# Optimization experiments

Hardware: AMD Instinct MI355X
Metric: run time of the kernel (lower is better)

## Reference

```python
import jax, jax.numpy as jnp
import numpy as np

D_MODEL = 5
NUM_PRED = 3
D_K = D_MODEL + NUM_PRED  # 8
HIDDEN = 128
GRID_LEN = 0.1
NUM_GRIDS = 100  # time_horizon / grid_length
SCALE = float(np.power(D_K, 0.5))
OH = np.eye(NUM_PRED, dtype=np.float32)
ONEHOT_M = jnp.asarray(OH[0])   # mental predicate 0
ONEHOT_A1 = jnp.asarray(OH[1])  # action predicate 1
ONEHOT_A2 = jnp.asarray(OH[2])  # action predicate 2


def time_emb(t):
    # positional-style embedding: even dims sin, odd dims cos (matches fast_time_embedding)
    i = jnp.arange(D_MODEL)
    ang = jnp.asarray(t)[..., None] / (10000.0 ** (2.0 * i / D_MODEL))
    return jnp.where(i % 2 == 0, jnp.sin(ang), jnp.cos(ang))


def setup_inputs() -> dict:
    key = jax.random.key(0)
    ks = jax.random.split(key, 11)
    B, L = 1024, 2048
    times_a1 = jnp.sort(jax.random.uniform(ks[0], (B, L)) * 10.0, axis=1)
    times_a2 = jnp.sort(jax.random.uniform(ks[1], (B, L)) * 10.0, axis=1)
    u = jax.random.uniform(ks[2], (B, NUM_GRIDS))
    s = 0.05
    return {
        'times_a1': times_a1,
        'times_a2': times_a2,
        'u': u,
        'W_ih': s * jax.random.normal(ks[3], (4 * HIDDEN, 21)),
        'W_hh': s * jax.random.normal(ks[4], (4 * HIDDEN, HIDDEN)),
        'b_ih': s * jax.random.normal(ks[5], (4 * HIDDEN,)),
        'b_hh': s * jax.random.normal(ks[6], (4 * HIDDEN,)),
        'w1': s * jax.random.normal(ks[7], (5, HIDDEN)),
        'b1': s * jax.random.normal(ks[8], (5,)),
        'w2': s * jax.random.normal(ks[9], (1, 5)),
        'b2': s * jax.random.normal(ks[10], (1,)),
    }


def _forward(times_a1, times_a2, u, W_ih, W_hh, b_ih, b_hh, w1, b1, w2, b2):
    B = times_a1.shape[0]
    # action event embeddings: [B, L, D_MODEL+NUM_PRED]; k = v = concat over action types
    e1 = jnp.concatenate([time_emb(times_a1), jnp.broadcast_to(ONEHOT_A1, times_a1.shape + (NUM_PRED,))], axis=-1)
    e2 = jnp.concatenate([time_emb(times_a2), jnp.broadcast_to(ONEHOT_A2, times_a2.shape + (NUM_PRED,))], axis=-1)
    kv = jnp.concatenate([e1, e2], axis=1)  # [B, 2L, 8]

    cur_times = (jnp.arange(NUM_GRIDS) + 1.0) * GRID_LEN  # [100]

    def step(carry, xs):
        hx, cx, last_time, has_event, dyn_time = carry
        cur_time, u_t = xs
        # query for mental predicate 0 at cur_time: [8]
        q = jnp.concatenate([time_emb(cur_time), ONEHOT_M])
        scores = jnp.einsum('d,bld->bl', q, kv) / SCALE
        attn = jax.nn.softmax(scores, axis=-1)
        att_out = jnp.einsum('bl,bld->bd', attn, kv)  # [B, 8]
        # mental embedding: zeros before first event, else time-emb of last event + one-hot
        m_emb = jnp.concatenate([time_emb(last_time), jnp.broadcast_to(ONEHOT_M, (B, NUM_PRED))], axis=-1)
        m_emb = jnp.where(has_event[:, None], m_emb, 0.0)
        dyn_time = dyn_time + GRID_LEN
        ct_emb = time_emb(dyn_time)  # [B, 5]
        x = jnp.concatenate([att_out, m_emb, ct_emb], axis=-1)  # [B, 21]
        # torch LSTMCell: gates ordered i, f, g, o
        gates = x @ W_ih.T + hx @ W_hh.T + b_ih + b_hh
        i_, f_, g_, o_ = jnp.split(gates, 4, axis=-1)
        cx = jax.nn.sigmoid(f_) * cx + jax.nn.sigmoid(i_) * jnp.tanh(g_)
        hx = jax.nn.sigmoid(o_) * jnp.tanh(cx)
        hz = jax.nn.sigmoid((hx @ w1.T + b1) @ w2.T + b2)[:, 0]  # [B]
        # bernoulli(prob) with pre-drawn uniform; single mental predicate -> index always 0
        event = u_t < hz
        last_time = jnp.where(event, cur_time, last_time)
        has_event = has_event | event
        dyn_time = jnp.where(event, 0.0, dyn_time)
        return (hx, cx, last_time, has_event, dyn_time), (hz, event)

    init = (
        jnp.zeros((B, HIDDEN)), jnp.zeros((B, HIDDEN)),
        jnp.zeros((B,)), jnp.zeros((B,), dtype=bool), jnp.zeros((B,)),
    )
    _, (hazard, events) = jax.lax.scan(step, init, (cur_times, u.T))
    return hazard, events  # [NUM_GRIDS, B], [NUM_GRIDS, B]


def reference(times_a1, times_a2, u, W_ih, W_hh, b_ih, b_hh, w1, b1, w2, b2):
    return _forward(times_a1, times_a2, u, W_ih, W_hh, b_ih, b_hh, w1, b1, w2, b2)
```

## Files before the change

### kernel.cpp

```cpp
#include <hip/hip_runtime.h>
#include <math.h>

#define BTOT 1024
#define LEN  2048
#define T    100
#define HID  128

#define C1 0.025118864315095794
#define C2 6.309573444801933e-04
#define C3 1.5848931924611134e-05
#define C4 3.9810717055349735e-07

#define TEMB(td) \
  float d0 = sinf((float)(td)); \
  float d1 = cosf((float)((td) * C1)); \
  float d2 = sinf((float)((td) * C2)); \
  float d3 = cosf((float)((td) * C3)); \
  float d4 = sinf((float)((td) * C4));

__device__ __forceinline__ float sig(float x) { return 1.0f / (1.0f + expf(-x)); }

template <int CTRL>
__device__ __forceinline__ float dppadd(float x) {
  int r = __builtin_amdgcn_update_dpp(0, __float_as_int(x), CTRL, 0xF, 0xF, false);
  return x + __int_as_float(r);
}
__device__ __forceinline__ float wred(float x) {
  x = dppadd<0xB1>(x);
  x = dppadd<0x4E>(x);
  x = dppadd<0x124>(x);
  x = dppadd<0x128>(x);
  x += __shfl_xor(x, 16);
  x += __shfl_xor(x, 32);
  return x;
}

__global__ __launch_bounds__(256)
__attribute__((amdgpu_waves_per_eu(4, 4)))
void attn_k(const float* __restrict__ ta1,
            const float* __restrict__ ta2,
            float* __restrict__ att) {
  const int b = blockIdx.x, tid = threadIdx.x;
  const int wave = tid >> 6, lane = tid & 63;

  __shared__ float qlds[T][8];
  __shared__ float strip[4][T][8];

  if (tid < T) {
    double ct = (double)(tid + 1) * 0.1;
    TEMB(ct);
    qlds[tid][0] = d0 * 0.35355339059327373f;
    qlds[tid][1] = d1 * 0.35355339059327373f;
    qlds[tid][2] = d2 * 0.35355339059327373f;
    qlds[tid][3] = d3 * 0.35355339059327373f;
    qlds[tid][4] = d4 * 0.35355339059327373f;
  }

#define E5(i) float e##i##_0, e##i##_1, e##i##_2, e##i##_3, e##i##_4;
  E5(0) E5(1) E5(2) E5(3) E5(4) E5(5) E5(6) E5(7)
  E5(8) E5(9) E5(10) E5(11) E5(12) E5(13) E5(14) E5(15)
#undef E5
#define STAGE(i, expr) { double td_ = (double)(expr); \
    e##i##_0 = sinf((float)td_); \
    e##i##_1 = cosf((float)(td_ * C1)); \
    e##i##_2 = sinf((float)(td_ * C2)); \
    e##i##_3 = cosf((float)(td_ * C3)); \
    e##i##_4 = sinf((float)(td_ * C4)); }
  STAGE(0,  ta1[b * LEN + tid +    0])
  STAGE(1,  ta1[b * LEN + tid +  256])
  STAGE(2,  ta1[b * LEN + tid +  512])
  STAGE(3,  ta1[b * LEN + tid +  768])
  STAGE(4,  ta1[b * LEN + tid + 1024])
  STAGE(5,  ta1[b * LEN + tid + 1280])
  STAGE(6,  ta1[b * LEN + tid + 1536])
  STAGE(7,  ta1[b * LEN + tid + 1792])
  STAGE(8,  ta2[b * LEN + tid +    0])
  STAGE(9,  ta2[b * LEN + tid +  256])
  STAGE(10, ta2[b * LEN + tid +  512])
  STAGE(11, ta2[b * LEN + tid +  768])
  STAGE(12, ta2[b * LEN + tid + 1024])
  STAGE(13, ta2[b * LEN + tid + 1280])
  STAGE(14, ta2[b * LEN + tid + 1536])
  STAGE(15, ta2[b * LEN + tid + 1792])
#undef STAGE
#define PIN5(i) asm volatile("" : "+v"(e##i##_0), "+v"(e##i##_1), \
    "+v"(e##i##_2), "+v"(e##i##_3), "+v"(e##i##_4));
  PIN5(0) PIN5(1) PIN5(2) PIN5(3) PIN5(4) PIN5(5) PIN5(6) PIN5(7)
  PIN5(8) PIN5(9) PIN5(10) PIN5(11) PIN5(12) PIN5(13) PIN5(14) PIN5(15)
#undef PIN5

  __syncthreads();

  for (int t = 0; t < T; t++) {
    const float4 qv = *(const float4*)&qlds[t][0];
    const float q4 = qlds[t][4];
    float Wx = 0.f, Wy = 0.f, Wz = 0.f, Ww = 0.f, W4 = 0.f, sA = 0.f, sB = 0.f;
#define EV(i, S) { \
    float s = fmaf(qv.x, e##i##_0, fmaf(qv.y, e##i##_1, \
              fmaf(qv.z, e##i##_2, fmaf(qv.w, e##i##_3, q4 * e##i##_4)))); \
    float e = __expf(s); S += e; \
    Wx = fmaf(e, e##i##_0, Wx); Wy = fmaf(e, e##i##_1, Wy); \
    Wz = fmaf(e, e##i##_2, Wz); Ww = fmaf(e, e##i##_3, Ww); \
    W4 = fmaf(e, e##i##_4, W4); }
    EV(0, sA) EV(1, sA) EV(2, sA) EV(3, sA)
    EV(4, sA) EV(5, sA) EV(6, sA) EV(7, sA)
    EV(8, sB) EV(9, sB) EV(10, sB) EV(11, sB)
    EV(12, sB) EV(13, sB) EV(14, sB) EV(15, sB)
#undef EV

    float r0 = wred(Wx), r1 = wred(Wy), r2 = wred(Wz), r3 = wred(Ww);
    float r4 = wred(W4), r5 = wred(sA), r6 = wred(sB);
    if (lane == 0) {
      *(float4*)&strip[wave][t][0] = make_float4(r0, r1, r2, r3);
      strip[wave][t][4] = r4; strip[wave][t][5] = r5; strip[wave][t][6] = r6;
    }
  }
  __syncthreads();

  if (tid < T) {
    float4 a0 = *(float4*)&strip[0][tid][0], b0 = *(float4*)&strip[0][tid][4];
    float4 a1 = *(float4*)&strip[1][tid][0], b1 = *(float4*)&strip[1][tid][4];
    float4 a2 = *(float4*)&strip[2][tid][0], b2 = *(float4*)&strip[2][tid][4];
    float4 a3 = *(float4*)&strip[3][tid][0], b3 = *(float4*)&strip[3][tid][4];
    float f0 = a0.x + a1.x + a2.x + a3.x;
    float f1 = a0.y + a1.y + a2.y + a3.y;
    float f2 = a0.z + a1.z + a2.z + a3.z;
    float f3 = a0.w + a1.w + a2.w + a3.w;
    float f4 = b0.x + b1.x + b2.x + b3.x;
    float f5 = b0.y + b1.y + b2.y + b3.y;
    float f6 = b0.z + b1.z + b2.z + b3.z;
    float inv = 1.0f / (f5 + f6);
    float* o8 = &att[(size_t)b * (T * 8) + (size_t)tid * 8];
    o8[0] = f0 * inv; o8[1] = f1 * inv; o8[2] = f2 * inv;
    o8[3] = f3 * inv; o8[4] = f4 * inv;
    o8[5] = 0.f; o8[6] = f5 * inv; o8[7] = f6 * inv;
  }
}

__device__ __forceinline__ float wcat(const float* Wih, const float* Whh, int r, int e) {
  return (e < 21) ? Wih[r * 21 + e] : (e < 24) ? 0.f : Whh[r * HID + e - 24];
}

__global__ __launch_bounds__(1024)
__attribute__((amdgpu_waves_per_eu(4, 4)))
void lstm_k(const float* __restrict__ att,
            const float* __restrict__ u,
            const float* __restrict__ Wih,
            const float* __restrict__ Whh,
            const float* __restrict__ bih,
            const float* __restrict__ bhh,
            const float* __restrict__ w1g,
            const float* __restrict__ b1g,
            const float* __restrict__ w2g,
            const float* __restrict__ b2g,
            float* __restrict__ out) {
  const int tid = threadIdx.x;
  const int bg = blockIdx.x * 4;
  const int r = tid >> 1, half = tid & 1;
  const int CB = 19 * half;
  const int ch = tid & 127;

  __shared__ float4 xb4[4 * 38];
  __shared__ float glf[4 * 512];
  __shared__ float red[8][5];
  __shared__ int stL[2][4], stD[2][4], stH[2][4];
  float* xbf = (float*)xb4;

  const int eb = 76 * half;
#define DECLW(c) float wr##c##_0 = wcat(Wih, Whh, r, eb + 4*(c) + 0), \
                       wr##c##_1 = wcat(Wih, Whh, r, eb + 4*(c) + 1), \
                       wr##c##_2 = wcat(Wih, Whh, r, eb + 4*(c) + 2), \
                       wr##c##_3 = wcat(Wih, Whh, r, eb + 4*(c) + 3);
  DECLW(0) DECLW(1) DECLW(2) DECLW(3) DECLW(4) DECLW(5) DECLW(6) DECLW(7)
  DECLW(8) DECLW(9) DECLW(10) DECLW(11) DECLW(12) DECLW(13) DECLW(14)
  DECLW(15) DECLW(16) DECLW(17) DECLW(18)
#undef DECLW
  float binit = half ? 0.f : (bih[r] + bhh[r]);

  float w1_0 = w1g[0*HID + ch], w1_1 = w1g[1*HID + ch], w1_2 = w1g[2*HID + ch],
        w1_3 = w1g[3*HID + ch], w1_4 = w1g[4*HID + ch];
  const float b1_0 = b1g[0], b1_1 = b1g[1], b1_2 = b1g[2], b1_3 = b1g[3], b1_4 = b1g[4];
  const float w2_0 = w2g[0], w2_1 = w2g[1], w2_2 = w2g[2], w2_3 = w2g[3], w2_4 = w2g[4];
  const float b2r = b2g[0];

#define PINW(c) asm volatile("" : "+v"(wr##c##_0), "+v"(wr##c##_1), \
    "+v"(wr##c##_2), "+v"(wr##c##_3));
  PINW(0) PINW(1) PINW(2) PINW(3) PINW(4) PINW(5) PINW(6) PINW(7)
  PINW(8) PINW(9) PINW(10) PINW(11) PINW(12) PINW(13) PINW(14)
  PINW(15) PINW(16) PINW(17) PINW(18)
#undef PINW
  asm volatile("" : "+v"(binit), "+v"(w1_0), "+v"(w1_1), "+v"(w1_2),
                    "+v"(w1_3), "+v"(w1_4));

  for (int i = tid; i < 4 * 152; i += 1024) xbf[i] = 0.f;
  if (tid < 4) { stL[0][tid] = 0; stD[0][tid] = 0; stH[0][tid] = 0; }
  float cx = 0.f;
  __syncthreads();

  if (tid < 32) {
    int b = tid >> 3, j = tid & 7;
    xbf[b * 152 + j] = att[(size_t)(bg + b) * (T * 8) + j];
  } else if (tid >= 64 && tid < 84) {
    int s = tid - 64, b = s / 5, j = s % 5;
    TEMB(0.1);
    xbf[b * 152 + 16 + j] = (j == 0) ? d0 : (j == 1) ? d1 : (j == 2) ? d2 : (j == 3) ? d3 : d4;
  }
  __syncthreads();

#define CALCEV(bb) \
    float z_ = b2r; \
    z_ = fmaf(w2_0, red[2*(bb)][0] + red[2*(bb)+1][0] + b1_0, z_); \
    z_ = fmaf(w2_1, red[2*(bb)][1] + red[2*(bb)+1][1] + b1_1, z_); \
    z_ = fmaf(w2_2, red[2*(bb)][2] + red[2*(bb)+1][2] + b1_2, z_); \
    z_ = fmaf(w2_3, red[2*(bb)][3] + red[2*(bb)+1][3] + b1_3, z_); \
    z_ = fmaf(w2_4, red[2*(bb)][4] + red[2*(bb)+1][4] + b1_4, z_); \
    float hz_ = 1.f / (1.f + expf(-z_)); \
    int ev_ = (u[(size_t)(bg + (bb)) * T + t] < hz_) ? 1 : 0; \
    int tb_ = t & 1; \
    int lastp_ = ev_ ? (t + 1) : stL[tb_][bb]; \
    int hasp_ = stH[tb_][bb] | ev_; \
    int dynp_ = ev_ ? 0 : (stD[tb_][bb] + 1);

  for (int t = 0; t < T; t++) {
    float a0 = binit, a1 = binit, a2 = binit, a3 = binit;
#define GB(c) { \
    float4 v0 = xb4[0*38 + CB + (c)], v1 = xb4[1*38 + CB + (c)]; \
    float4 v2 = xb4[2*38 + CB + (c)], v3 = xb4[3*38 + CB + (c)]; \
    a0 = fmaf(wr##c##_0, v0.x, a0); a0 = fmaf(wr##c##_1, v0.y, a0); \
    a0 = fmaf(wr##c##_2, v0.z, a0); a0 = fmaf(wr##c##_3, v0.w, a0); \
    a1 = fmaf(wr##c##_0, v1.x, a1); a1 = fmaf(wr##c##_1, v1.y, a1); \
    a1 = fmaf(wr##c##_2, v1.z, a1); a1 = fmaf(wr##c##_3, v1.w, a1); \
    a2 = fmaf(wr##c##_0, v2.x, a2); a2 = fmaf(wr##c##_1, v2.y, a2); \
    a2 = fmaf(wr##c##_2, v2.z, a2); a2 = fmaf(wr##c##_3, v2.w, a2); \
    a3 = fmaf(wr##c##_0, v3.x, a3); a3 = fmaf(wr##c##_1, v3.y, a3); \
    a3 = fmaf(wr##c##_2, v3.z, a3); a3 = fmaf(wr##c##_3, v3.w, a3); }
    GB(0) GB(1) GB(2) GB(3) GB(4) GB(5) GB(6) GB(7) GB(8) GB(9)
    GB(10) GB(11) GB(12) GB(13) GB(14) GB(15) GB(16) GB(17) GB(18)
#undef GB
    a0 = dppadd<0xB1>(a0); a1 = dppadd<0xB1>(a1);
    a2 = dppadd<0xB1>(a2); a3 = dppadd<0xB1>(a3);
    if (!half) {
      glf[0*512 + r] = a0; glf[1*512 + r] = a1;
      glf[2*512 + r] = a2; glf[3*512 + r] = a3;
    }
    __syncthreads();

    if (tid < 512) {
      int b = tid >> 7;
      float gi = glf[b*512 + ch], gf = glf[b*512 + 128 + ch],
            gg = glf[b*512 + 256 + ch], go = glf[b*512 + 384 + ch];
      cx = sig(gf) * cx + sig(gi) * tanhf(gg);
      float hn = sig(go) * tanhf(cx);
      xbf[b * 152 + 24 + ch] = hn;
      float p0 = wred(w1_0 * hn), p1 = wred(w1_1 * hn), p2 = wred(w1_2 * hn),
            p3 = wred(w1_3 * hn), p4 = wred(w1_4 * hn);
      if ((tid & 63) == 0) {
        int w = tid >> 6;
        red[w][0] = p0; red[w][1] = p1; red[w][2] = p2;
        red[w][3] = p3; red[w][4] = p4;
      }
    }
    __syncthreads();

    if (tid < 4) {
      int b = tid;
      CALCEV(b);
      out[(size_t)t * BTOT + bg + b] = hz_;
      out[(size_t)T * BTOT + (size_t)t * BTOT + bg + b] = ev_ ? 1.f : 0.f;
      stL[tb_ ^ 1][b] = lastp_; stH[tb_ ^ 1][b] = hasp_; stD[tb_ ^ 1][b] = dynp_;
    }
    if (t < T - 1) {
      if (tid < 32) {
        int b = tid >> 3, j = tid & 7;
        xbf[b * 152 + j] = att[(size_t)(bg + b) * (T * 8) + (size_t)(t + 1) * 8 + j];
      } else if (tid < 52) {
        int s = tid - 32, b = s / 5, j = s % 5;
        CALCEV(b);
        float v = 0.f;
        if (hasp_) {
          double td = (double)lastp_ * 0.1;
          TEMB(td);
          v = (j == 0) ? d0 : (j == 1) ? d1 : (j == 2) ? d2 : (j == 3) ? d3 : d4;
        }
        xbf[b * 152 + 8 + j] = v;
      } else if (tid < 64) {
        int s = tid - 52, b = s / 3, j = s % 3;
        CALCEV(b);
        xbf[b * 152 + 13 + j] = (j == 0 && hasp_) ? 1.f : 0.f;
      } else if (tid < 84) {
        int s = tid - 64, b = s / 5, j = s % 5;
        CALCEV(b);
        double td = (double)(dynp_ + 1) * 0.1;
        TEMB(td);
        xbf[b * 152 + 16 + j] =
            (j == 0) ? d0 : (j == 1) ? d1 : (j == 2) ? d2 : (j == 3) ? d3 : d4;
      }
    }
    __syncthreads();
  }
#undef CALCEV
}

extern "C" void kernel_launch(void* const* d_in, const int* in_sizes, int n_in,
                              void* d_out, int out_size, void* d_ws, size_t ws_size,
                              hipStream_t stream) {
  const float* ta1 = (const float*)d_in[0];
  const float* ta2 = (const float*)d_in[1];
  const float* u   = (const float*)d_in[2];
  const float* Wih = (const float*)d_in[3];
  const float* Whh = (const float*)d_in[4];
  const float* bih = (const float*)d_in[5];
  const float* bhh = (const float*)d_in[6];
  const float* w1  = (const float*)d_in[7];
  const float* b1  = (const float*)d_in[8];
  const float* w2  = (const float*)d_in[9];
  const float* b2  = (const float*)d_in[10];
  float* out = (float*)d_out;
  float* att = (float*)d_ws;

  attn_k<<<dim3(BTOT), dim3(256), 0, stream>>>(ta1, ta2, att);
  lstm_k<<<dim3(BTOT / 4), dim3(1024), 0, stream>>>(att, u, Wih, Whh, bih, bhh,
                                                    w1, b1, w2, b2, out);
}
```

Measured before the change: 836.9 us.

## Restructure LSTM step so each thread owns all four gates of one unit

```diff
diff --git a/kernel.cpp b/kernel.cpp
--- a/kernel.cpp
+++ b/kernel.cpp
@@ -19,6 +19,9 @@
   float d4 = sinf((float)((td) * C4));
 
 __device__ __forceinline__ float sig(float x) { return 1.0f / (1.0f + expf(-x)); }
+
+using v2f = __attribute__((ext_vector_type(2))) float;
+__device__ __forceinline__ v2f mkv2(float a, float b) { v2f r; r.x = a; r.y = b; return r; }
 
 template <int CTRL>
 __device__ __forceinline__ float dppadd(float x) {
@@ -34,9 +37,9 @@
   x += __shfl_xor(x, 32);
   return x;
 }
-
-__global__ __launch_bounds__(256)
-__attribute__((amdgpu_waves_per_eu(4, 4)))
+#define RED8(x) { x = dppadd<0xB1>(x); x = dppadd<0x4E>(x); x = dppadd<0x141>(x); }
+
+__global__ __attribute__((amdgpu_flat_work_group_size(256, 256), amdgpu_waves_per_eu(4, 4)))
 void attn_k(const float* __restrict__ ta1,
             const float* __restrict__ ta2,
             float* __restrict__ att) {
@@ -137,12 +140,16 @@
   }
 }
 
-__device__ __forceinline__ float wcat(const float* Wih, const float* Whh, int r, int e) {
-  return (e < 21) ? Wih[r * 21 + e] : (e < 24) ? 0.f : Whh[r * HID + e - 24];
-}
-
-__global__ __launch_bounds__(1024)
-__attribute__((amdgpu_waves_per_eu(4, 4)))
+__device__ __forceinline__ float wc(const float* Wih, const float* Whh, int row, int e) {
+  return (e < 21) ? Wih[row * 21 + e]
+       : (e < 24) ? 0.f
+       : (e < 152) ? Whh[row * HID + (e - 24)]
+       : 0.f;
+}
+
+#define XE(tb, b, e) (((tb) * 4 + (b)) * 160 + (e))
+
+__global__ __attribute__((amdgpu_flat_work_group_size(1024, 1024), amdgpu_waves_per_eu(4, 4)))
 void lstm_k(const float* __restrict__ att,
             const float* __restrict__ u,
             const float* __restrict__ Wih,
@@ -156,109 +163,115 @@
             float* __restrict__ out) {
   const int tid = threadIdx.x;
   const int bg = blockIdx.x * 4;
-  const int r = tid >> 1, half = tid & 1;
-  const int CB = 19 * half;
-  const int ch = tid & 127;
-
-  __shared__ float4 xb4[4 * 38];
-  __shared__ float glf[4 * 512];
-  __shared__ float red[8][5];
+  const int q = tid >> 3, s = tid & 7;
+  const int wave = tid >> 6, lane = tid & 63;
+
+  __shared__ float4 xls4[2][4][40];
+  __shared__ float4 red4[2][4][4];
   __shared__ int stL[2][4], stD[2][4], stH[2][4];
-  float* xbf = (float*)xb4;
-
-  const int eb = 76 * half;
-#define DECLW(c) float wr##c##_0 = wcat(Wih, Whh, r, eb + 4*(c) + 0), \
-                       wr##c##_1 = wcat(Wih, Whh, r, eb + 4*(c) + 1), \
-                       wr##c##_2 = wcat(Wih, Whh, r, eb + 4*(c) + 2), \
-                       wr##c##_3 = wcat(Wih, Whh, r, eb + 4*(c) + 3);
-  DECLW(0) DECLW(1) DECLW(2) DECLW(3) DECLW(4) DECLW(5) DECLW(6) DECLW(7)
-  DECLW(8) DECLW(9) DECLW(10) DECLW(11) DECLW(12) DECLW(13) DECLW(14)
-  DECLW(15) DECLW(16) DECLW(17) DECLW(18)
-#undef DECLW
-  float binit = half ? 0.f : (bih[r] + bhh[r]);
-
-  float w1_0 = w1g[0*HID + ch], w1_1 = w1g[1*HID + ch], w1_2 = w1g[2*HID + ch],
-        w1_3 = w1g[3*HID + ch], w1_4 = w1g[4*HID + ch];
-  const float b1_0 = b1g[0], b1_1 = b1g[1], b1_2 = b1g[2], b1_3 = b1g[3], b1_4 = b1g[4];
-  const float w2_0 = w2g[0], w2_1 = w2g[1], w2_2 = w2g[2], w2_3 = w2g[3], w2_4 = w2g[4];
-  const float b2r = b2g[0];
-
-#define PINW(c) asm volatile("" : "+v"(wr##c##_0), "+v"(wr##c##_1), \
-    "+v"(wr##c##_2), "+v"(wr##c##_3));
-  PINW(0) PINW(1) PINW(2) PINW(3) PINW(4) PINW(5) PINW(6) PINW(7)
-  PINW(8) PINW(9) PINW(10) PINW(11) PINW(12) PINW(13) PINW(14)
-  PINW(15) PINW(16) PINW(17) PINW(18)
-#undef PINW
-  asm volatile("" : "+v"(binit), "+v"(w1_0), "+v"(w1_1), "+v"(w1_2),
-                    "+v"(w1_3), "+v"(w1_4));
-
-  for (int i = tid; i < 4 * 152; i += 1024) xbf[i] = 0.f;
+  float* xf = (float*)xls4;
+  float* rf = (float*)red4;
+
+#define WD(g, c) v2f w##g##_##c = mkv2(wc(Wih, Whh, q + 128 * (g), 20 * s + 2 * (c)), \
+                                       wc(Wih, Whh, q + 128 * (g), 20 * s + 2 * (c) + 1));
+#define WR(g) WD(g, 0) WD(g, 1) WD(g, 2) WD(g, 3) WD(g, 4) WD(g, 5) WD(g, 6) WD(g, 7) WD(g, 8) WD(g, 9)
+  WR(0) WR(1) WR(2) WR(3)
+#undef WR
+#undef WD
+#define PW(g) asm volatile("" : "+v"(w##g##_0), "+v"(w##g##_1), "+v"(w##g##_2), \
+    "+v"(w##g##_3), "+v"(w##g##_4), "+v"(w##g##_5), "+v"(w##g##_6), "+v"(w##g##_7), \
+    "+v"(w##g##_8), "+v"(w##g##_9));
+  PW(0) PW(1) PW(2) PW(3)
+#undef PW
+
+  float bb0 = bih[q] + bhh[q];
+  float bb1 = bih[q + 128] + bhh[q + 128];
+  float bb2 = bih[q + 256] + bhh[q + 256];
+  float bb3 = bih[q + 384] + bhh[q + 384];
+  float wv = 0.f;
+#pragma unroll
+  for (int j = 0; j < 5; j++) wv = fmaf(w2g[j], w1g[j * HID + q], wv);
+  float hconst = b2g[0];
+#pragma unroll
+  for (int j = 0; j < 5; j++) hconst = fmaf(w2g[j], b1g[j], hconst);
+  asm volatile("" : "+v"(bb0), "+v"(bb1), "+v"(bb2), "+v"(bb3), "+v"(wv));
+  float cx0 = 0.f, cx1 = 0.f, cx2 = 0.f, cx3 = 0.f;
+
+  for (int i = tid; i < 2 * 4 * 160; i += 1024) xf[i] = 0.f;
   if (tid < 4) { stL[0][tid] = 0; stD[0][tid] = 0; stH[0][tid] = 0; }
-  float cx = 0.f;
   __syncthreads();
 
   if (tid < 32) {
     int b = tid >> 3, j = tid & 7;
-    xbf[b * 152 + j] = att[(size_t)(bg + b) * (T * 8) + j];
+    xf[XE(0, b, j)] = att[(size_t)(bg + b) * (T * 8) + j];
   } else if (tid >= 64 && tid < 84) {
-    int s = tid - 64, b = s / 5, j = s % 5;
+    int s2 = tid - 64, b = s2 / 5, j = s2 % 5;
     TEMB(0.1);
-    xbf[b * 152 + 16 + j] = (j == 0) ? d0 : (j == 1) ? d1 : (j == 2) ? d2 : (j == 3) ? d3 : d4;
+    xf[XE(0, b, 16 + j)] = (j == 0) ? d0 : (j == 1) ? d1 : (j == 2) ? d2 : (j == 3) ? d3 : d4;
   }
   __syncthreads();
 
+#define FMS(g, a) \
+  a = __builtin_elementwise_fma(w##g##_0, mkv2(u0.x, u0.y), a); \
+  a = __builtin_elementwise_fma(w##g##_1, mkv2(u0.z, u0.w), a); \
+  a = __builtin_elementwise_fma(w##g##_2, mkv2(u1.x, u1.y), a); \
+  a = __builtin_elementwise_fma(w##g##_3, mkv2(u1.z, u1.w), a); \
+  a = __builtin_elementwise_fma(w##g##_4, mkv2(u2.x, u2.y), a); \
+  a = __builtin_elementwise_fma(w##g##_5, mkv2(u2.z, u2.w), a); \
+  a = __builtin_elementwise_fma(w##g##_6, mkv2(u3.x, u3.y), a); \
+  a = __builtin_elementwise_fma(w##g##_7, mkv2(u3.z, u3.w), a); \
+  a = __builtin_elementwise_fma(w##g##_8, mkv2(u4.x, u4.y), a); \
+  a = __builtin_elementwise_fma(w##g##_9, mkv2(u4.z, u4.w), a);
+
+#define BATCH(b, s0, s1, s2n, s3n) { \
+  const float4* xp = &xls4[tb][b][s * 5]; \
+  float4 u0 = xp[0], u1 = xp[1], u2 = xp[2], u3 = xp[3], u4 = xp[4]; \
+  v2f a0 = mkv2(0.f, 0.f), a1 = a0, a2 = a0, a3 = a0; \
+  FMS(0, a0) FMS(1, a1) FMS(2, a2) FMS(3, a3) \
+  s0 = a0.x + a0.y; s1 = a1.x + a1.y; s2n = a2.x + a2.y; s3n = a3.x + a3.y; }
+
+#define CELL(b, cxv) { \
+  float gi = g0##b + bb0, gf = g1##b + bb1, gG = g2##b + bb2, go = g3##b + bb3; \
+  cxv = sig(gf) * cxv + sig(gi) * tanhf(gG); \
+  float hn = sig(go) * tanhf(cxv); \
+  xf[XE(tb1, b, 24 + q)] = hn; \
+  pb##b = wv * hn; }
+
 #define CALCEV(bb) \
-    float z_ = b2r; \
-    z_ = fmaf(w2_0, red[2*(bb)][0] + red[2*(bb)+1][0] + b1_0, z_); \
-    z_ = fmaf(w2_1, red[2*(bb)][1] + red[2*(bb)+1][1] + b1_1, z_); \
-    z_ = fmaf(w2_2, red[2*(bb)][2] + red[2*(bb)+1][2] + b1_2, z_); \
-    z_ = fmaf(w2_3, red[2*(bb)][3] + red[2*(bb)+1][3] + b1_3, z_); \
-    z_ = fmaf(w2_4, red[2*(bb)][4] + red[2*(bb)+1][4] + b1_4, z_); \
+    float4 r0 = red4[tb][bb][0], r1 = red4[tb][bb][1], \
+           r2 = red4[tb][bb][2], r3 = red4[tb][bb][3]; \
+    float z_ = hconst + (((r0.x + r0.y) + (r0.z + r0.w)) + ((r1.x + r1.y) + (r1.z + r1.w))) \
+                      + (((r2.x + r2.y) + (r2.z + r2.w)) + ((r3.x + r3.y) + (r3.z + r3.w))); \
     float hz_ = 1.f / (1.f + expf(-z_)); \
     int ev_ = (u[(size_t)(bg + (bb)) * T + t] < hz_) ? 1 : 0; \
-    int tb_ = t & 1; \
-    int lastp_ = ev_ ? (t + 1) : stL[tb_][bb]; \
-    int hasp_ = stH[tb_][bb] | ev_; \
-    int dynp_ = ev_ ? 0 : (stD[tb_][bb] + 1);
+    int lastp_ = ev_ ? (t + 1) : stL[tb][bb]; \
+    int hasp_ = stH[tb][bb] | ev_; \
+    int dynp_ = ev_ ? 0 : (stD[tb][bb] + 1);
 
   for (int t = 0; t < T; t++) {
-    float a0 = binit, a1 = binit, a2 = binit, a3 = binit;
-#define GB(c) { \
-    float4 v0 = xb4[0*38 + CB + (c)], v1 = xb4[1*38 + CB + (c)]; \
-    float4 v2 = xb4[2*38 + CB + (c)], v3 = xb4[3*38 + CB + (c)]; \
-    a0 = fmaf(wr##c##_0, v0.x, a0); a0 = fmaf(wr##c##_1, v0.y, a0); \
-    a0 = fmaf(wr##c##_2, v0.z, a0); a0 = fmaf(wr##c##_3, v0.w, a0); \
-    a1 = fmaf(wr##c##_0, v1.x, a1); a1 = fmaf(wr##c##_1, v1.y, a1); \
-    a1 = fmaf(wr##c##_2, v1.z, a1); a1 = fmaf(wr##c##_3, v1.w, a1); \
-    a2 = fmaf(wr##c##_0, v2.x, a2); a2 = fmaf(wr##c##_1, v2.y, a2); \
-    a2 = fmaf(wr##c##_2, v2.z, a2); a2 = fmaf(wr##c##_3, v2.w, a2); \
-    a3 = fmaf(wr##c##_0, v3.x, a3); a3 = fmaf(wr##c##_1, v3.y, a3); \
-    a3 = fmaf(wr##c##_2, v3.z, a3); a3 = fmaf(wr##c##_3, v3.w, a3); }
-    GB(0) GB(1) GB(2) GB(3) GB(4) GB(5) GB(6) GB(7) GB(8) GB(9)
-    GB(10) GB(11) GB(12) GB(13) GB(14) GB(15) GB(16) GB(17) GB(18)
-#undef GB
-    a0 = dppadd<0xB1>(a0); a1 = dppadd<0xB1>(a1);
-    a2 = dppadd<0xB1>(a2); a3 = dppadd<0xB1>(a3);
-    if (!half) {
-      glf[0*512 + r] = a0; glf[1*512 + r] = a1;
-      glf[2*512 + r] = a2; glf[3*512 + r] = a3;
-    }
-    __syncthreads();
-
-    if (tid < 512) {
-      int b = tid >> 7;
-      float gi = glf[b*512 + ch], gf = glf[b*512 + 128 + ch],
-            gg = glf[b*512 + 256 + ch], go = glf[b*512 + 384 + ch];
-      cx = sig(gf) * cx + sig(gi) * tanhf(gg);
-      float hn = sig(go) * tanhf(cx);
-      xbf[b * 152 + 24 + ch] = hn;
-      float p0 = wred(w1_0 * hn), p1 = wred(w1_1 * hn), p2 = wred(w1_2 * hn),
-            p3 = wred(w1_3 * hn), p4 = wred(w1_4 * hn);
-      if ((tid & 63) == 0) {
-        int w = tid >> 6;
-        red[w][0] = p0; red[w][1] = p1; red[w][2] = p2;
-        red[w][3] = p3; red[w][4] = p4;
-      }
+    const int tb = t & 1, tb1 = tb ^ 1;
+
+    float g00, g10, g20, g30, g01, g11, g21, g31,
+          g02, g12, g22, g32, g03, g13, g23, g33;
+    BATCH(0, g00, g10, g20, g30)
+    BATCH(1, g01, g11, g21, g31)
+    BATCH(2, g02, g12, g22, g32)
+    BATCH(3, g03, g13, g23, g33)
+    RED8(g00) RED8(g10) RED8(g20) RED8(g30)
+    RED8(g01) RED8(g11) RED8(g21) RED8(g31)
+    RED8(g02) RED8(g12) RED8(g22) RED8(g32)
+    RED8(g03) RED8(g13) RED8(g23) RED8(g33)
+
+    float pb0 = 0.f, pb1 = 0.f, pb2 = 0.f, pb3 = 0.f;
+    if (s == 0) {
+      CELL(0, cx0) CELL(1, cx1) CELL(2, cx2) CELL(3, cx3)
+    }
+    pb0 = wred(pb0); pb1 = wred(pb1); pb2 = wred(pb2); pb3 = wred(pb3);
+    if (lane == 0) {
+      rf[(tb * 4 + 0) * 16 + wave] = pb0;
+      rf[(tb * 4 + 1) * 16 + wave] = pb1;
+      rf[(tb * 4 + 2) * 16 + wave] = pb2;
+      rf[(tb * 4 + 3) * 16 + wave] = pb3;
     }
     __syncthreads();
 
@@ -267,14 +280,14 @@
       CALCEV(b);
       out[(size_t)t * BTOT + bg + b] = hz_;
       out[(size_t)T * BTOT + (size_t)t * BTOT + bg + b] = ev_ ? 1.f : 0.f;
-      stL[tb_ ^ 1][b] = lastp_; stH[tb_ ^ 1][b] = hasp_; stD[tb_ ^ 1][b] = dynp_;
+      stL[tb1][b] = lastp_; stH[tb1][b] = hasp_; stD[tb1][b] = dynp_;
     }
     if (t < T - 1) {
       if (tid < 32) {
         int b = tid >> 3, j = tid & 7;
-        xbf[b * 152 + j] = att[(size_t)(bg + b) * (T * 8) + (size_t)(t + 1) * 8 + j];
+        xf[XE(tb1, b, j)] = att[(size_t)(bg + b) * (T * 8) + (size_t)(t + 1) * 8 + j];
       } else if (tid < 52) {
-        int s = tid - 32, b = s / 5, j = s % 5;
+        int s2 = tid - 32, b = s2 / 5, j = s2 % 5;
         CALCEV(b);
         float v = 0.f;
         if (hasp_) {
@@ -282,23 +295,26 @@
           TEMB(td);
           v = (j == 0) ? d0 : (j == 1) ? d1 : (j == 2) ? d2 : (j == 3) ? d3 : d4;
         }
-        xbf[b * 152 + 8 + j] = v;
+        xf[XE(tb1, b, 8 + j)] = v;
       } else if (tid < 64) {
-        int s = tid - 52, b = s / 3, j = s % 3;
+        int s2 = tid - 52, b = s2 / 3, j = s2 % 3;
         CALCEV(b);
-        xbf[b * 152 + 13 + j] = (j == 0 && hasp_) ? 1.f : 0.f;
+        xf[XE(tb1, b, 13 + j)] = (j == 0 && hasp_) ? 1.f : 0.f;
       } else if (tid < 84) {
-        int s = tid - 64, b = s / 5, j = s % 5;
+        int s2 = tid - 64, b = s2 / 5, j = s2 % 5;
         CALCEV(b);
         double td = (double)(dynp_ + 1) * 0.1;
         TEMB(td);
-        xbf[b * 152 + 16 + j] =
+        xf[XE(tb1, b, 16 + j)] =
             (j == 0) ? d0 : (j == 1) ? d1 : (j == 2) ? d2 : (j == 3) ? d3 : d4;
       }
     }
     __syncthreads();
   }
 #undef CALCEV
+#undef CELL
+#undef BATCH
+#undef FMS
 }
 
 extern "C" void kernel_launch(void* const* d_in, const int* in_sizes, int n_in,
```

New measurement: 1.246 ms. 48.9% more time.
